# Optimization experiments

Hardware: AMD Instinct MI355X
Metric: run time of the kernel (lower is better)

## Reference

```python
import jax, jax.numpy as jnp
import numpy as np

# Standard SMPL kinematic tree (parent of joint i); root parent is -1.
PARENTS = [-1, 0, 0, 0, 1, 2, 3, 4, 5, 6, 7, 8, 9, 9, 9, 12, 13, 14, 16, 17, 18, 19, 20, 21]
NUM_JOINTS = 24
NUM_VERTICES = 6890
NUM_BETAS = 10
UNIT_FACTOR = 1.0  # unit='m'


def rotvec2mat(r):
    """Rodrigues formula. r: (..., 3) -> (..., 3, 3)."""
    theta = jnp.linalg.norm(r, axis=-1, keepdims=True)            # (..., 1)
    safe_theta = jnp.where(theta < 1e-8, 1.0, theta)
    axis = r / safe_theta
    x, y, z = axis[..., 0], axis[..., 1], axis[..., 2]
    zeros = jnp.zeros_like(x)
    K = jnp.stack([zeros, -z, y, z, zeros, -x, -y, x, zeros], axis=-1)
    K = K.reshape(r.shape[:-1] + (3, 3))
    t = theta[..., None]                                          # (..., 1, 1)
    eye = jnp.eye(3, dtype=r.dtype)
    return eye + jnp.sin(t) * K + (1.0 - jnp.cos(t)) * (K @ K)


def setup_inputs() -> dict:
    key = jax.random.key(0)
    ks = jax.random.split(key, 9)
    B = 1024
    pose_rotvecs = 0.3 * jax.random.normal(ks[0], (B, NUM_JOINTS, 3), jnp.float32)
    shape_betas = jax.random.normal(ks[1], (B, NUM_BETAS), jnp.float32)
    trans = jax.random.normal(ks[2], (B, 3), jnp.float32)
    v_template = jax.random.normal(ks[3], (NUM_VERTICES, 3), jnp.float32)
    shapedirs = 0.01 * jax.random.normal(ks[4], (NUM_VERTICES, 3, NUM_BETAS), jnp.float32)
    posedirs = 0.01 * jax.random.normal(ks[5], (NUM_VERTICES, 3, (NUM_JOINTS - 1) * 9), jnp.float32)
    J_template = jax.random.normal(ks[6], (NUM_JOINTS, 3), jnp.float32)
    J_shapedirs = 0.01 * jax.random.normal(ks[7], (NUM_JOINTS, 3, NUM_BETAS), jnp.float32)
    w = jax.random.uniform(ks[8], (NUM_VERTICES, NUM_JOINTS), jnp.float32)
    weights = w / jnp.sum(w, axis=-1, keepdims=True)  # skinning weights: rows sum to 1
    return dict(pose_rotvecs=pose_rotvecs, shape_betas=shape_betas, trans=trans,
                v_template=v_template, shapedirs=shapedirs, posedirs=posedirs,
                J_template=J_template, J_shapedirs=J_shapedirs, weights=weights)


def reference(pose_rotvecs, shape_betas, trans, v_template, shapedirs, posedirs,
              J_template, J_shapedirs, weights):
    B = pose_rotvecs.shape[0]
    parent_idx = jnp.asarray(PARENTS[1:], dtype=jnp.int32)  # (J-1,)

    # Parent-relative rotation matrices from rotation vectors.
    rel_rotmats = rotvec2mat(pose_rotvecs)                  # (B, J, 3, 3)

    # Kinematic chain: compose global rotations along the tree (J=24, fixed small loop).
    glob_list = [rel_rotmats[:, 0]]
    for i in range(1, NUM_JOINTS):
        glob_list.append(glob_list[PARENTS[i]] @ rel_rotmats[:, i])
    glob_rotmats = jnp.stack(glob_list, axis=1)             # (B, J, 3, 3)

    eye = jnp.broadcast_to(jnp.eye(3, dtype=rel_rotmats.dtype), (B, 1, 3, 3))
    parent_glob = jnp.concatenate([eye, glob_rotmats[:, parent_idx]], axis=1)  # (B, J, 3, 3)

    # Shaped joint locations (kid_factor = 0 default -> term vanishes).
    j = J_template + jnp.einsum('jcs,bs->bjc', J_shapedirs, shape_betas)       # (B, J, 3)
    j_parent = jnp.concatenate([jnp.zeros((B, 1, 3), j.dtype), j[:, parent_idx]], axis=1)
    bones = j - j_parent
    rotated_bones = jnp.einsum('bjCc,bjc->bjC', parent_glob, bones)

    pos_list = [j[:, 0]]
    for i in range(1, NUM_JOINTS):
        pos_list.append(pos_list[PARENTS[i]] + rotated_bones[:, i])
    glob_positions = jnp.stack(pos_list, axis=1)            # (B, J, 3)

    # Blendshapes: shape + pose correctives (kid term zero).
    pose_feature = rel_rotmats[:, 1:].reshape(B, (NUM_JOINTS - 1) * 9)
    v_posed = (v_template
               + jnp.einsum('vcp,bp->bvc', shapedirs, shape_betas)
               + jnp.einsum('vcp,bp->bvc', posedirs, pose_feature))            # (B, V, 3)

    # Linear blend skinning.
    translations = glob_positions - jnp.einsum('bjCc,bjc->bjC', glob_rotmats, j)  # (B, J, 3)
    blended_rot = jnp.einsum('vj,bjCc->bvCc', weights, glob_rotmats)              # (B, V, 3, 3)
    vertices = (jnp.einsum('bvCc,bvc->bvC', blended_rot, v_posed)
                + jnp.einsum('vj,bjc->bvc', weights, translations))               # (B, V, 3)

    joints = (glob_positions + trans[:, None]) * UNIT_FACTOR
    vertices = (vertices + trans[:, None]) * UNIT_FACTOR
    return joints, vertices, glob_rotmats
```

## Files before the change

### kernel.cpp

```cpp
#include <hip/hip_runtime.h>
#include <math.h>

#define NJ 24
#define NV 6890
#define NB 10
#define KREAL 217
#define KP 224
#define NVT 432

typedef __attribute__((ext_vector_type(8))) short bf16x8;
typedef __attribute__((ext_vector_type(8))) unsigned short u16x8;
typedef __attribute__((ext_vector_type(4))) float f32x4;

__device__ __forceinline__ unsigned short f2bf(float x) {
    unsigned int u = __float_as_uint(x);
    u += 0x7fffu + ((u >> 16) & 1u);
    return (unsigned short)(u >> 16);
}
__device__ __forceinline__ float bf2f(unsigned short h) {
    return __uint_as_float(((unsigned int)h) << 16);
}

__device__ __constant__ int c_path[NJ][9] = {
  {0,0,0,0,0,0,0,0,0},
  {0,1,0,0,0,0,0,0,0},
  {0,2,0,0,0,0,0,0,0},
  {0,3,0,0,0,0,0,0,0},
  {0,1,4,0,0,0,0,0,0},
  {0,2,5,0,0,0,0,0,0},
  {0,3,6,0,0,0,0,0,0},
  {0,1,4,7,0,0,0,0,0},
  {0,2,5,8,0,0,0,0,0},
  {0,3,6,9,0,0,0,0,0},
  {0,1,4,7,10,0,0,0,0},
  {0,2,5,8,11,0,0,0,0},
  {0,3,6,9,12,0,0,0,0},
  {0,3,6,9,13,0,0,0,0},
  {0,3,6,9,14,0,0,0,0},
  {0,3,6,9,12,15,0,0,0},
  {0,3,6,9,13,16,0,0,0},
  {0,3,6,9,14,17,0,0,0},
  {0,3,6,9,13,16,18,0,0},
  {0,3,6,9,14,17,19,0,0},
  {0,3,6,9,13,16,18,20,0},
  {0,3,6,9,14,17,19,21,0},
  {0,3,6,9,13,16,18,20,22},
  {0,3,6,9,14,17,19,21,23}};
__device__ __constant__ int c_plen[NJ] = {1,2,2,2,3,3,3,4,4,4,5,5,5,5,5,6,6,6,7,7,8,8,9,9};

__global__ __launch_bounds__(256)
void pack_kernel(const float* __restrict__ shapedirs, const float* __restrict__ posedirs,
                 unsigned short* __restrict__ dirsF)
{
    __shared__ unsigned short tile[16][3][240];
    const int t = threadIdx.x;
    const int vtg = blockIdx.x;

    for (int idx = t; idx < 16 * 3 * KP; idx += 256) {
        const int v_l = idx / (3 * KP);
        const int rem = idx - v_l * (3 * KP);
        const int c = rem / KP;
        const int k = rem - c * KP;
        const int v = vtg * 16 + v_l;
        float val = 0.f;
        if (v < NV && k < KREAL)
            val = (k < NB) ? shapedirs[(size_t)v * 30 + c * NB + k]
                           : posedirs[(size_t)v * 621 + c * 207 + (k - NB)];
        tile[v_l][c][k] = f2bf(val);
    }
    __syncthreads();

    const int lane = t & 63;
    const int w = t >> 6;
    const int kg = lane >> 4;
    const int vsub = lane & 15;
    for (int j2 = w; j2 < 21; j2 += 4) {
        const int kt = j2 / 3;
        const int c = j2 - kt * 3;
        const u16x8 o = *(const u16x8*)&tile[vsub][c][kt * 32 + kg * 8];
        *(u16x8*)&dirsF[(((size_t)(kt * 3 + c) * NVT + vtg) * 64 + lane) * 8] = o;
    }
}

__global__ __launch_bounds__(64)
void prep_kernel(const float* __restrict__ pose, const float* __restrict__ betas,
                 const float* __restrict__ trans, const float* __restrict__ J_template,
                 const float* __restrict__ J_shapedirs,
                 float* __restrict__ joints_out, float* __restrict__ glob_out,
                 unsigned short* __restrict__ AF, unsigned short* __restrict__ AFL,
                 unsigned short* __restrict__ coeffF, int B)
{
    const int b = blockIdx.x;
    const int t = threadIdx.x;
    __shared__ float s_beta[NB];
    __shared__ float s_rel[NJ][9];
    __shared__ float s_glob[NJ][9];
    __shared__ float s_j[NJ][3];
    __shared__ float s_A[NJ][12];

    if (t < NB) s_beta[t] = betas[b * NB + t];
    __syncthreads();

    if (t < NJ) {
        float rx = pose[b * 72 + t * 3 + 0];
        float ry = pose[b * 72 + t * 3 + 1];
        float rz = pose[b * 72 + t * 3 + 2];
        float th = sqrtf(rx * rx + ry * ry + rz * rz);
        float safe = (th < 1e-8f) ? 1.0f : th;
        float ax = rx / safe, ay = ry / safe, az = rz / safe;
        float s = sinf(th), c = cosf(th), omc = 1.0f - c;
        float aa = ax * ax + ay * ay + az * az;
        float K[9] = {0.f, -az, ay, az, 0.f, -ax, -ay, ax, 0.f};
        float A2[9] = {ax*ax - aa, ax*ay,      ax*az,
                       ay*ax,      ay*ay - aa, ay*az,
                       az*ax,      az*ay,      az*az - aa};
        #pragma unroll
        for (int r = 0; r < 3; ++r)
            #pragma unroll
            for (int cc = 0; cc < 3; ++cc)
                s_rel[t][r * 3 + cc] = ((r == cc) ? 1.0f : 0.0f)
                                     + s * K[r * 3 + cc] + omc * A2[r * 3 + cc];
        #pragma unroll
        for (int cc = 0; cc < 3; ++cc) {
            float acc = J_template[t * 3 + cc];
            #pragma unroll
            for (int q = 0; q < NB; ++q)
                acc = fmaf(J_shapedirs[(t * 3 + cc) * NB + q], s_beta[q], acc);
            s_j[t][cc] = acc;
        }
    }
    __syncthreads();

    if (t < NJ) {
        const int L = c_plen[t];
        float G[9];
        #pragma unroll
        for (int e = 0; e < 9; ++e) G[e] = s_rel[0][e];
        for (int sIdx = 1; sIdx < L; ++sIdx) {
            const int p = c_path[t][sIdx];
            float Tn[9];
            #pragma unroll
            for (int r = 0; r < 3; ++r)
                #pragma unroll
                for (int cc = 0; cc < 3; ++cc)
                    Tn[r * 3 + cc] = G[r * 3 + 0] * s_rel[p][0 * 3 + cc]
                                   + G[r * 3 + 1] * s_rel[p][1 * 3 + cc]
                                   + G[r * 3 + 2] * s_rel[p][2 * 3 + cc];
            #pragma unroll
            for (int e = 0; e < 9; ++e) G[e] = Tn[e];
        }
        #pragma unroll
        for (int e = 0; e < 9; ++e) s_glob[t][e] = G[e];
        #pragma unroll
        for (int e = 0; e < 9; ++e) glob_out[(size_t)b * 216 + t * 9 + e] = G[e];
    }
    __syncthreads();

    if (t < NJ) {
        const int L = c_plen[t];
        float px = s_j[0][0], py = s_j[0][1], pz = s_j[0][2];
        for (int sIdx = 1; sIdx < L; ++sIdx) {
            const int pk = c_path[t][sIdx];
            const int pp = c_path[t][sIdx - 1];
            float bx = s_j[pk][0] - s_j[pp][0];
            float by = s_j[pk][1] - s_j[pp][1];
            float bz = s_j[pk][2] - s_j[pp][2];
            px += s_glob[pp][0] * bx + s_glob[pp][1] * by + s_glob[pp][2] * bz;
            py += s_glob[pp][3] * bx + s_glob[pp][4] * by + s_glob[pp][5] * bz;
            pz += s_glob[pp][6] * bx + s_glob[pp][7] * by + s_glob[pp][8] * bz;
        }
        const float tx = trans[b * 3 + 0], ty = trans[b * 3 + 1], tz = trans[b * 3 + 2];
        joints_out[(size_t)b * 72 + t * 3 + 0] = px + tx;
        joints_out[(size_t)b * 72 + t * 3 + 1] = py + ty;
        joints_out[(size_t)b * 72 + t * 3 + 2] = pz + tz;
        const float jx = s_j[t][0], jy = s_j[t][1], jz = s_j[t][2];
        float T0 = px - (s_glob[t][0] * jx + s_glob[t][1] * jy + s_glob[t][2] * jz) + tx;
        float T1 = py - (s_glob[t][3] * jx + s_glob[t][4] * jy + s_glob[t][5] * jz) + ty;
        float T2 = pz - (s_glob[t][6] * jx + s_glob[t][7] * jy + s_glob[t][8] * jz) + tz;
        s_A[t][0]  = s_glob[t][0]; s_A[t][1]  = s_glob[t][1]; s_A[t][2]  = s_glob[t][2]; s_A[t][3]  = T0;
        s_A[t][4]  = s_glob[t][3]; s_A[t][5]  = s_glob[t][4]; s_A[t][6]  = s_glob[t][5]; s_A[t][7]  = T1;
        s_A[t][8]  = s_glob[t][6]; s_A[t][9]  = s_glob[t][7]; s_A[t][10] = s_glob[t][8]; s_A[t][11] = T2;
    }
    __syncthreads();

    const int btg = b >> 4, bl = b & 15, bt_ = (b >> 4) & 3;
    for (int k = t; k < KP; k += 64) {
        float val;
        if (k < NB) val = s_beta[k];
        else if (k < KREAL) { const int p2 = k - NB; val = s_rel[1 + p2 / 9][p2 % 9]; }
        else val = 0.f;
        const int kt = k >> 5, kg = (k >> 3) & 3, i = k & 7;
        coeffF[(((size_t)kt * (B >> 4) + btg) * 64 + kg * 16 + bl) * 8 + i] = f2bf(val);
    }
    for (int idx = t; idx < 12 * 32; idx += 64) {
        const int e = idx >> 5, jj = idx & 31, kg = jj >> 3, i = jj & 7;
        const float val = (jj < NJ) ? s_A[jj][e] : 0.f;
        AF[((((size_t)(b >> 6) * 12 + e) * 4 + bt_) * 64 + kg * 16 + bl) * 8 + i] = f2bf(val);
    }
    for (int idx = t; idx < 3 * 32; idx += 64) {
        const int et = idx >> 5, jj = idx & 31, kg = jj >> 3, i = jj & 7;
        const float val = (jj < NJ) ? s_A[jj][et * 4 + 3] : 0.f;
        const unsigned short hi = f2bf(val);
        AFL[((((size_t)(b >> 6) * 3 + et) * 4 + bt_) * 64 + kg * 16 + bl) * 8 + i]
            = f2bf(val - bf2f(hi));
    }
}

__global__ __launch_bounds__(256)
void vert_kernel(const float4* __restrict__ dirsF, const float4* __restrict__ coeffF,
                 const float4* __restrict__ AF, const float4* __restrict__ AFL,
                 const float* __restrict__ v_template, const float* __restrict__ weights,
                 float* __restrict__ vert_out, int B)
{
    __shared__ float smem[6336];
    const int tid  = threadIdx.x;
    const int lane = tid & 63;
    const int w    = __builtin_amdgcn_readfirstlane(tid >> 6);
    const int vt   = w;
    const int vb4  = blockIdx.y * 4;
    const int bblk = blockIdx.x;
    const int nbt  = B >> 4;

    f32x4 acc[3][4];
    #pragma unroll
    for (int c = 0; c < 3; ++c)
        #pragma unroll
        for (int bt = 0; bt < 4; ++bt) {
            acc[c][bt][0] = 0.f; acc[c][bt][1] = 0.f; acc[c][bt][2] = 0.f; acc[c][bt][3] = 0.f;
        }

    for (int kt = 0; kt < 7; ++kt) {
        __syncthreads();
        #pragma unroll
        for (int s = 0; s < 3; ++s) {
            const int row = s * 256 + tid;
            const int ch = row >> 6, l2 = row & 63;
            *(float4*)&smem[row * 4] =
                dirsF[((size_t)(kt * 3 + (ch >> 2)) * NVT + vb4 + (ch & 3)) * 64 + l2];
        }
        __syncthreads();
        bf16x8 bq[4];
        #pragma unroll
        for (int bt = 0; bt < 4; ++bt)
            bq[bt] = *(const bf16x8*)&coeffF[((size_t)kt * nbt + bblk * 4 + bt) * 64 + lane];
        #pragma unroll
        for (int c = 0; c < 3; ++c) {
            const bf16x8 a = *(const bf16x8*)&smem[((c * 4 + vt) * 64 + lane) * 4];
            #pragma unroll
            for (int bt = 0; bt < 4; ++bt)
                acc[c][bt] = __builtin_amdgcn_mfma_f32_16x16x32_bf16(a, bq[bt], acc[c][bt], 0, 0, 0);
        }
    }

    const int vrow0 = (vb4 + vt) * 16 + ((lane >> 4) << 2);
    #pragma unroll
    for (int c = 0; c < 3; ++c) {
        float tv[4];
        #pragma unroll
        for (int r = 0; r < 4; ++r) {
            const int v = vrow0 + r;
            tv[r] = (v < NV) ? v_template[(size_t)v * 3 + c] : 0.f;
        }
        #pragma unroll
        for (int bt = 0; bt < 4; ++bt) {
            acc[c][bt][0] += tv[0]; acc[c][bt][1] += tv[1];
            acc[c][bt][2] += tv[2]; acc[c][bt][3] += tv[3];
        }
    }

    bf16x8 wh, wl;
    {
        const int vA = (vb4 + vt) * 16 + (lane & 15);
        const int kg = lane >> 4;
        if (kg < 3 && vA < NV) {
            const float* wp = weights + (size_t)vA * NJ + kg * 8;
            #pragma unroll
            for (int i = 0; i < 8; ++i) {
                const float val = wp[i];
                const unsigned short hi = f2bf(val);
                wh[i] = (short)hi;
                wl[i] = (short)f2bf(val - bf2f(hi));
            }
        } else {
            #pragma unroll
            for (int i = 0; i < 8; ++i) { wh[i] = 0; wl[i] = 0; }
        }
    }

    __syncthreads();

    f32x4 zero; zero[0] = 0.f; zero[1] = 0.f; zero[2] = 0.f; zero[3] = 0.f;
    const int vglob = vb4 * 16 + lane;

    for (int p = 0; p < 2; ++p) {
        if (p) __syncthreads();
        #pragma unroll
        for (int half = 0; half < 2; ++half) {
            const int bt = 2 * p + half;
            #pragma unroll
            for (int C = 0; C < 3; ++C) {
                const size_t baseT  = (((size_t)bblk * 12 + (C * 4 + 3)) * 4 + bt) * 64 + lane;
                const size_t baseTL = (((size_t)bblk * 3 + C) * 4 + bt) * 64 + lane;
                const bf16x8 ATh = *(const bf16x8*)&AF[baseT];
                const bf16x8 ATl = *(const bf16x8*)&AFL[baseTL];
                f32x4 out = __builtin_amdgcn_mfma_f32_16x16x32_bf16(wl, ATh, zero, 0, 0, 0);
                out = __builtin_amdgcn_mfma_f32_16x16x32_bf16(wh, ATl, out, 0, 0, 0);
                out = __builtin_amdgcn_mfma_f32_16x16x32_bf16(wh, ATh, out, 0, 0, 0);
                #pragma unroll
                for (int q = 0; q < 3; ++q) {
                    const size_t baseR = (((size_t)bblk * 12 + (C * 4 + q)) * 4 + bt) * 64 + lane;
                    const bf16x8 ARh = *(const bf16x8*)&AF[baseR];
                    f32x4 rr = __builtin_amdgcn_mfma_f32_16x16x32_bf16(wl, ARh, zero, 0, 0, 0);
                    rr = __builtin_amdgcn_mfma_f32_16x16x32_bf16(wh, ARh, rr, 0, 0, 0);
                    out[0] = fmaf(rr[0], acc[q][bt][0], out[0]);
                    out[1] = fmaf(rr[1], acc[q][bt][1], out[1]);
                    out[2] = fmaf(rr[2], acc[q][bt][2], out[2]);
                    out[3] = fmaf(rr[3], acc[q][bt][3], out[3]);
                }
                const int b32 = half * 16 + (lane & 15);
                const int vl  = vt * 16 + ((lane >> 4) << 2);
                smem[(C * 32 + b32) * 66 + vl + 0] = out[0];
                smem[(C * 32 + b32) * 66 + vl + 1] = out[1];
                smem[(C * 32 + b32) * 66 + vl + 2] = out[2];
                smem[(C * 32 + b32) * 66 + vl + 3] = out[3];
            }
        }
        __syncthreads();

        if (vglob < NV) {
            #pragma unroll
            for (int i = 0; i < 8; ++i) {
                const int b32 = w * 8 + i;
                const int b = bblk * 64 + p * 32 + b32;
                const float o0 = smem[(0 * 32 + b32) * 66 + lane];
                const float o1 = smem[(1 * 32 + b32) * 66 + lane];
                const float o2 = smem[(2 * 32 + b32) * 66 + lane];
                const size_t off = (size_t)b * (NV * 3) + (size_t)vglob * 3;
                vert_out[off + 0] = o0;
                vert_out[off + 1] = o1;
                vert_out[off + 2] = o2;
            }
        }
    }
}

extern "C" void kernel_launch(void* const* d_in, const int* in_sizes, int n_in,
                              void* d_out, int out_size, void* d_ws, size_t ws_size,
                              hipStream_t stream) {
    const float* pose        = (const float*)d_in[0];
    const float* betas       = (const float*)d_in[1];
    const float* trans       = (const float*)d_in[2];
    const float* v_template  = (const float*)d_in[3];
    const float* shapedirs   = (const float*)d_in[4];
    const float* posedirs    = (const float*)d_in[5];
    const float* J_template  = (const float*)d_in[6];
    const float* J_shapedirs = (const float*)d_in[7];
    const float* weights     = (const float*)d_in[8];
    const int B = in_sizes[0] / 72;

    float* out = (float*)d_out;
    float* joints_out = out;
    float* vert_out   = out + (size_t)B * 72;
    float* glob_out   = out + (size_t)B * 72 + (size_t)B * NV * 3;

    char* ws = (char*)d_ws;
    const size_t coeff_bytes = (size_t)7 * (B >> 4) * 64 * 16;
    const size_t af_bytes    = (size_t)(B >> 6) * 12 * 4 * 64 * 16;
    const size_t afl_bytes   = (size_t)(B >> 6) * 3 * 4 * 64 * 16;
    unsigned short* coeffF = (unsigned short*)ws;
    unsigned short* AF     = (unsigned short*)(ws + coeff_bytes);
    unsigned short* AFL    = (unsigned short*)(ws + coeff_bytes + af_bytes);
    unsigned short* dirsF  = (unsigned short*)(ws + coeff_bytes + af_bytes + afl_bytes);

    pack_kernel<<<dim3(NVT), 256, 0, stream>>>(shapedirs, posedirs, dirsF);
    prep_kernel<<<dim3(B), 64, 0, stream>>>(pose, betas, trans, J_template, J_shapedirs,
                                            joints_out, glob_out, AF, AFL, coeffF, B);
    vert_kernel<<<dim3(B / 64, 108), 256, 0, stream>>>((const float4*)dirsF, (const float4*)coeffF,
                                                       (const float4*)AF, (const float4*)AFL,
                                                       v_template, weights, vert_out, B);
}
```

Before: 223.0 us.

## Prefetch next dirs tile into registers and coalesce vertex output stores

The global loads of the next k-tile of blend-shape directions are now issued into registers before the current tile is consumed, so load latency overlaps the MFMA work instead of stalling between barriers. The vertex output write-out is also reorganised: threads cooperatively read the staged shared-memory tile and write contiguous float2 pairs along the flattened (vertex, coord) axis, replacing three strided scalar stores per vertex. This costs extra registers for the prefetched float4s and integer div/mod index math in the store loop, which may affect occupancy.

```diff
diff --git a/kernel.cpp b/kernel.cpp
--- a/kernel.cpp
+++ b/kernel.cpp
@@ -229,14 +229,23 @@
             acc[c][bt][0] = 0.f; acc[c][bt][1] = 0.f; acc[c][bt][2] = 0.f; acc[c][bt][3] = 0.f;
         }
 
+    const int row0 = tid, row1 = tid + 256, row2 = tid + 512;
+    const int ch0 = row0 >> 6, l20 = row0 & 63;
+    const int ch1 = row1 >> 6, l21 = row1 & 63;
+    const int ch2 = row2 >> 6, l22 = row2 & 63;
+    float4 nxt0 = dirsF[((size_t)(ch0 >> 2) * NVT + vb4 + (ch0 & 3)) * 64 + l20];
+    float4 nxt1 = dirsF[((size_t)(ch1 >> 2) * NVT + vb4 + (ch1 & 3)) * 64 + l21];
+    float4 nxt2 = dirsF[((size_t)(ch2 >> 2) * NVT + vb4 + (ch2 & 3)) * 64 + l22];
+
     for (int kt = 0; kt < 7; ++kt) {
         __syncthreads();
-        #pragma unroll
-        for (int s = 0; s < 3; ++s) {
-            const int row = s * 256 + tid;
-            const int ch = row >> 6, l2 = row & 63;
-            *(float4*)&smem[row * 4] =
-                dirsF[((size_t)(kt * 3 + (ch >> 2)) * NVT + vb4 + (ch & 3)) * 64 + l2];
+        *(float4*)&smem[row0 * 4] = nxt0;
+        *(float4*)&smem[row1 * 4] = nxt1;
+        *(float4*)&smem[row2 * 4] = nxt2;
+        if (kt < 6) {
+            nxt0 = dirsF[((size_t)((kt + 1) * 3 + (ch0 >> 2)) * NVT + vb4 + (ch0 & 3)) * 64 + l20];
+            nxt1 = dirsF[((size_t)((kt + 1) * 3 + (ch1 >> 2)) * NVT + vb4 + (ch1 & 3)) * 64 + l21];
+            nxt2 = dirsF[((size_t)((kt + 1) * 3 + (ch2 >> 2)) * NVT + vb4 + (ch2 & 3)) * 64 + l22];
         }
         __syncthreads();
         bf16x8 bq[4];
@@ -290,7 +299,6 @@
     __syncthreads();
 
     f32x4 zero; zero[0] = 0.f; zero[1] = 0.f; zero[2] = 0.f; zero[3] = 0.f;
-    const int vglob = vb4 * 16 + lane;
 
     for (int p = 0; p < 2; ++p) {
         if (p) __syncthreads();
@@ -327,18 +335,24 @@
         }
         __syncthreads();
 
-        if (vglob < NV) {
-            #pragma unroll
-            for (int i = 0; i < 8; ++i) {
-                const int b32 = w * 8 + i;
-                const int b = bblk * 64 + p * 32 + b32;
-                const float o0 = smem[(0 * 32 + b32) * 66 + lane];
-                const float o1 = smem[(1 * 32 + b32) * 66 + lane];
-                const float o2 = smem[(2 * 32 + b32) * 66 + lane];
-                const size_t off = (size_t)b * (NV * 3) + (size_t)vglob * 3;
-                vert_out[off + 0] = o0;
-                vert_out[off + 1] = o1;
-                vert_out[off + 2] = o2;
+        #pragma unroll
+        for (int it = 0; it < 12; ++it) {
+            const int flat2 = it * 256 + tid;
+            const int brow = flat2 / 96;
+            const int o2 = flat2 - brow * 96;
+            const int j0 = o2 * 2;
+            const int vl0 = j0 / 3, c0 = j0 - vl0 * 3;
+            const int j1 = j0 + 1;
+            const int vl1 = j1 / 3, c1 = j1 - vl1 * 3;
+            const float x = smem[(c0 * 32 + brow) * 66 + vl0];
+            const float y = smem[(c1 * 32 + brow) * 66 + vl1];
+            const int vg1 = vb4 * 16 + vl1;
+            const int b = bblk * 64 + p * 32 + brow;
+            float* dst = vert_out + (size_t)b * (NV * 3) + (size_t)vb4 * 48 + j0;
+            if (vg1 < NV) {
+                *(float2*)dst = make_float2(x, y);
+            } else if (vb4 * 16 + vl0 < NV) {
+                dst[0] = x;
             }
         }
     }
```

Result: faster. 205.6 us (-7.8%).
